# Optimization experiments

Measured on AMD Instinct MI355X. Metric: run time of the kernel, lower is better.

The kernel has to match this reference:

```python
import jax, jax.numpy as jnp
import numpy as np

TOPK_INC = 20  # top-k vertices per mention that form a hyperedge (torch.topk(attention_a, 20))
TOPK_OUT = 2   # top-k node reps concatenated into the output (torch.topk(X_score, k=2))


def _indicator_from_rows(att, idx):
    # att: [N, N], idx: [A] int. Rows with idx == 0 are skipped, as in the original loop.
    N = att.shape[0]
    rows = att[idx]                                   # [A, N] gather of attention rows
    _, top = jax.lax.top_k(rows, TOPK_INC)            # [A, TOPK_INC]
    mask = (idx != 0).astype(att.dtype)               # [A]
    vals = jnp.broadcast_to(mask[:, None], top.shape).reshape(-1)
    # scatter-max builds the 0/1 incidence vector (multiple mentions OR together)
    return jnp.zeros((N,), att.dtype).at[top.reshape(-1)].max(vals)  # [N]


def _forward_one(h, att, a_idx, b_idx, spk, W_w, W_b, S_w, S_b):
    # h: [N, H], att: [N, N], spk: [N] (single speaker row since speak_num == 1 -> E = 3)
    a_ind = _indicator_from_rows(att, a_idx)
    b_ind = _indicator_from_rows(att, b_idx)
    Hyper0 = jnp.stack([a_ind, b_ind, spk], axis=0)   # [E, N] binary incidence
    Dv = 1.0 / jnp.sqrt(Hyper0.sum(axis=0) + 1.0)     # sqrt(inverse(diag(Dv) + I)) diagonal, [N]
    De = 1.0 / jnp.sqrt(Hyper0.sum(axis=1))           # sqrt(inverse(diag(De))) diagonal, [E]
    Hyper = Hyper0 @ att                              # [E, N]  (dropout is identity in eval)
    Hyper_att = jax.nn.softmax(Hyper, axis=-1)        # F.softmax over last dim for 2D input
    Hyper_prime = Hyper_att @ h                       # [E, H]
    w = jax.nn.softmax(Hyper_prime @ W_w.T + W_b, axis=0)[:, 0]  # [E]
    # A = diag(Dv) @ Hyper0.T @ diag(w) @ diag(De) @ Hyper @ diag(Dv); X = A @ h.
    # Associate as M @ (K @ h) to avoid materializing the [N, N] matrix A.
    K = (w * De)[:, None] * Hyper * Dv[None, :]       # [E, N]
    M = Hyper0.T * Dv[:, None]                        # [N, E]
    X = M @ (K @ h)                                   # [N, H]
    score = (X @ S_w.T + S_b)[:, 0]                   # [N]
    _, top = jax.lax.top_k(score, TOPK_OUT)           # [2]
    return X[top].reshape(-1)                         # [2*H]


def setup_inputs() -> dict:
    key = jax.random.key(0)
    B, N, H, A = 32, 1024, 768, 8
    ks = jax.random.split(key, 8)
    inp = jax.random.normal(ks[0], (B, N, H), dtype=jnp.float32)
    word_att = jax.random.uniform(ks[1], (B, 1, N, N), dtype=jnp.float32)
    a_idx = jax.random.randint(ks[2], (B, A), 0, N)
    b_idx = jax.random.randint(ks[3], (B, A), 0, N)
    speak_num = jnp.ones((B, 1), dtype=jnp.int64 if jax.config.jax_enable_x64 else jnp.int32)
    speak_all = jax.random.randint(ks[4], (B, 3, N), 0, 2).astype(jnp.float32)
    W_w = jax.random.normal(ks[5], (1, H), dtype=jnp.float32) * (1.0 / np.sqrt(H))
    W_b = jnp.zeros((1,), dtype=jnp.float32)
    score_w = jax.random.normal(ks[6], (1, H), dtype=jnp.float32) * (1.0 / np.sqrt(H))
    score_b = jnp.zeros((1,), dtype=jnp.float32)
    return {"input": inp, "word_att": word_att, "a_idx": a_idx, "b_idx": b_idx,
            "speak_num": speak_num, "speak_all": speak_all,
            "W_w": W_w, "W_b": W_b, "score_w": score_w, "score_b": score_b}


def reference(input, word_att, a_idx, b_idx, speak_num, speak_all, W_w, W_b, score_w, score_b):
    # speak_num is all ones by construction -> exactly one speaker hyperedge per sample (E = 3)
    att = word_att[:, 0]           # [B, N, N]
    spk = speak_all[:, 0]          # [B, N]
    f = jax.vmap(_forward_one, in_axes=(0, 0, 0, 0, 0, None, None, None, None))
    return f(input, att, a_idx, b_idx, spk, W_w, W_b, score_w, score_b)  # [B, 2*H]
```

## Files before the change

### kernel.cpp

```cpp
#include <hip/hip_runtime.h>
#include <math.h>

#define B_ 32
#define N_ 1024
#define H_ 768
#define A_ 8
#define TOPK_ 20

__device__ __forceinline__ float wsum(float x) {
#pragma unroll
    for (int off = 32; off > 0; off >>= 1) x += __shfl_xor(x, off);
    return x;
}

__global__ __launch_bounds__(1024) void k1_ind(
    const float* __restrict__ att, const int* __restrict__ a_idx,
    const int* __restrict__ b_idx, const float* __restrict__ speak_all,
    float* __restrict__ aind, float* __restrict__ bind,
    float* __restrict__ Dv, float* __restrict__ De)
{
    const int b = blockIdx.x;
    const int tid = threadIdx.x;
    const int w = tid >> 6, lane = tid & 63;
    __shared__ float s_ind[2][N_];
    __shared__ float s_red[3][16];

    s_ind[0][tid] = 0.f;
    s_ind[1][tid] = 0.f;
    __syncthreads();

    const int which = w >> 3;
    const int r = w & 7;
    const int idx = which ? b_idx[b * A_ + r] : a_idx[b * A_ + r];
    if (idx != 0) {
        const float* row = att + ((size_t)b * N_ + idx) * N_;
        float v[16];
#pragma unroll
        for (int k = 0; k < 16; ++k) v[k] = row[(k << 6) + lane];
        float* dst = s_ind[which];
        for (int t = 0; t < TOPK_; ++t) {
            float bv = v[0]; int bk = 0;
#pragma unroll
            for (int k = 1; k < 16; ++k)
                if (v[k] > bv) { bv = v[k]; bk = k; }
            int bc = (bk << 6) + lane;
#pragma unroll
            for (int off = 32; off > 0; off >>= 1) {
                float ov = __shfl_xor(bv, off);
                int oc = __shfl_xor(bc, off);
                if (ov > bv || (ov == bv && oc < bc)) { bv = ov; bc = oc; }
            }
            if (lane == 0) dst[bc] = 1.f;
            if (lane == (bc & 63)) v[bc >> 6] = -INFINITY;
        }
    }
    __syncthreads();

    const float sa = s_ind[0][tid], sb = s_ind[1][tid];
    const float ss = speak_all[(size_t)b * 3 * N_ + tid];
    aind[b * N_ + tid] = sa;
    bind[b * N_ + tid] = sb;
    Dv[b * N_ + tid] = 1.f / sqrtf(sa + sb + ss + 1.f);

    float p[3] = {sa, sb, ss};
#pragma unroll
    for (int e = 0; e < 3; ++e) {
        float x = wsum(p[e]);
        if (lane == 0) s_red[e][w] = x;
    }
    __syncthreads();
    if (tid < 3) {
        float s = 0.f;
        for (int i = 0; i < 16; ++i) s += s_red[tid][i];
        De[b * 3 + tid] = 1.f / sqrtf(s);
    }
}

__global__ __launch_bounds__(256) void k2_hyper(
    const float* __restrict__ att, const float* __restrict__ aind,
    const float* __restrict__ bind, const float* __restrict__ speak_all,
    float* __restrict__ Hyper)
{
    const int b = blockIdx.y;
    const int col0 = blockIdx.x * 32;
    const int tid = threadIdx.x;
    const int cx = tid & 7, ry = tid >> 3;
    __shared__ float lds[256 * 13];
    float* w0 = lds;
    float* w1 = lds + N_;
    float* w2 = lds + 2 * N_;

    for (int n = tid; n < N_; n += 256) {
        w0[n] = aind[b * N_ + n];
        w1[n] = bind[b * N_ + n];
        w2[n] = speak_all[(size_t)b * 3 * N_ + n];
    }
    __syncthreads();

    float a0x=0,a0y=0,a0z=0,a0w=0, a1x=0,a1y=0,a1z=0,a1w=0, a2x=0,a2y=0,a2z=0,a2w=0;
    const float* base = att + (size_t)b * N_ * N_ + col0 + cx * 4;
    for (int n = ry; n < N_; n += 32) {
        const float x0 = w0[n], x1 = w1[n], x2 = w2[n];
        if (x0 == 0.f && x1 == 0.f && x2 == 0.f) continue;
        const float4 v = *(const float4*)(base + (size_t)n * N_);
        a0x += x0*v.x; a0y += x0*v.y; a0z += x0*v.z; a0w += x0*v.w;
        a1x += x1*v.x; a1y += x1*v.y; a1z += x1*v.z; a1w += x1*v.w;
        a2x += x2*v.x; a2y += x2*v.y; a2z += x2*v.z; a2w += x2*v.w;
    }
    __syncthreads();

    float vals[12] = {a0x,a0y,a0z,a0w, a1x,a1y,a1z,a1w, a2x,a2y,a2z,a2w};
    float* scr = lds;
#pragma unroll
    for (int k = 0; k < 12; ++k) scr[tid * 13 + k] = vals[k];
    __syncthreads();
    for (int s = 16; s > 0; s >>= 1) {
        if (ry < s) {
#pragma unroll
            for (int k = 0; k < 12; ++k)
                scr[tid * 13 + k] += scr[(tid + s * 8) * 13 + k];
        }
        __syncthreads();
    }
    if (ry == 0) {
#pragma unroll
        for (int e = 0; e < 3; ++e)
#pragma unroll
            for (int j = 0; j < 4; ++j)
                Hyper[(size_t)(b * 3 + e) * N_ + col0 + cx * 4 + j] = scr[tid * 13 + e * 4 + j];
    }
}

__global__ __launch_bounds__(256) void k4_ug(
    const float* __restrict__ h, const float* __restrict__ Hyper,
    const float* __restrict__ Dv, float* __restrict__ U, float* __restrict__ G)
{
    const int b = blockIdx.y;
    const int col0 = blockIdx.x * 32;
    const int tid = threadIdx.x;
    const int cx = tid & 7, ry = tid >> 3;
    const int lane = tid & 63, wv = tid >> 6;
    __shared__ float lds[256 * 25];
    float* sH = lds;
    float* sDv = lds + 3 * N_;
    float* rscr = lds + 4 * N_;

    for (int n = tid; n < N_; n += 256) {
        sDv[n] = Dv[b * N_ + n];
#pragma unroll
        for (int e = 0; e < 3; ++e)
            sH[e * N_ + n] = Hyper[(size_t)(b * 3 + e) * N_ + n];
    }
    __syncthreads();

    float m0 = -INFINITY, m1 = -INFINITY, m2 = -INFINITY;
    for (int n = tid; n < N_; n += 256) {
        m0 = fmaxf(m0, sH[n]); m1 = fmaxf(m1, sH[N_ + n]); m2 = fmaxf(m2, sH[2 * N_ + n]);
    }
#pragma unroll
    for (int off = 32; off > 0; off >>= 1) {
        m0 = fmaxf(m0, __shfl_xor(m0, off));
        m1 = fmaxf(m1, __shfl_xor(m1, off));
        m2 = fmaxf(m2, __shfl_xor(m2, off));
    }
    if (lane == 0) { rscr[wv * 3 + 0] = m0; rscr[wv * 3 + 1] = m1; rscr[wv * 3 + 2] = m2; }
    __syncthreads();
    m0 = fmaxf(fmaxf(rscr[0], rscr[3]), fmaxf(rscr[6], rscr[9]));
    m1 = fmaxf(fmaxf(rscr[1], rscr[4]), fmaxf(rscr[7], rscr[10]));
    m2 = fmaxf(fmaxf(rscr[2], rscr[5]), fmaxf(rscr[8], rscr[11]));
    __syncthreads();
    float s0 = 0.f, s1 = 0.f, s2 = 0.f;
    for (int n = tid; n < N_; n += 256) {
        s0 += expf(sH[n] - m0); s1 += expf(sH[N_ + n] - m1); s2 += expf(sH[2 * N_ + n] - m2);
    }
    s0 = wsum(s0); s1 = wsum(s1); s2 = wsum(s2);
    if (lane == 0) { rscr[wv * 3 + 0] = s0; rscr[wv * 3 + 1] = s1; rscr[wv * 3 + 2] = s2; }
    __syncthreads();
    const float iZ0 = 1.f / (rscr[0] + rscr[3] + rscr[6] + rscr[9]);
    const float iZ1 = 1.f / (rscr[1] + rscr[4] + rscr[7] + rscr[10]);
    const float iZ2 = 1.f / (rscr[2] + rscr[5] + rscr[8] + rscr[11]);
    __syncthreads();

    float u0x=0,u0y=0,u0z=0,u0w=0, u1x=0,u1y=0,u1z=0,u1w=0, u2x=0,u2y=0,u2z=0,u2w=0;
    float g0x=0,g0y=0,g0z=0,g0w=0, g1x=0,g1y=0,g1z=0,g1w=0, g2x=0,g2y=0,g2z=0,g2w=0;
    const float* base = h + (size_t)b * N_ * H_ + col0 + cx * 4;
    for (int n = ry; n < N_; n += 32) {
        const float H0 = sH[n], H1 = sH[N_ + n], H2 = sH[2 * N_ + n];
        const float dv = sDv[n];
        const float w0 = expf(H0 - m0) * iZ0;
        const float w1 = expf(H1 - m1) * iZ1;
        const float w2 = expf(H2 - m2) * iZ2;
        const float gg0 = H0 * dv, gg1 = H1 * dv, gg2 = H2 * dv;
        const float4 v = *(const float4*)(base + (size_t)n * H_);
        u0x += w0*v.x; u0y += w0*v.y; u0z += w0*v.z; u0w += w0*v.w;
        u1x += w1*v.x; u1y += w1*v.y; u1z += w1*v.z; u1w += w1*v.w;
        u2x += w2*v.x; u2y += w2*v.y; u2z += w2*v.z; u2w += w2*v.w;
        g0x += gg0*v.x; g0y += gg0*v.y; g0z += gg0*v.z; g0w += gg0*v.w;
        g1x += gg1*v.x; g1y += gg1*v.y; g1z += gg1*v.z; g1w += gg1*v.w;
        g2x += gg2*v.x; g2y += gg2*v.y; g2z += gg2*v.z; g2w += gg2*v.w;
    }
    __syncthreads();

    float vals[24] = {u0x,u0y,u0z,u0w, u1x,u1y,u1z,u1w, u2x,u2y,u2z,u2w,
                      g0x,g0y,g0z,g0w, g1x,g1y,g1z,g1w, g2x,g2y,g2z,g2w};
    float* scr = lds;
#pragma unroll
    for (int k = 0; k < 24; ++k) scr[tid * 25 + k] = vals[k];
    __syncthreads();
    for (int s = 16; s > 0; s >>= 1) {
        if (ry < s) {
#pragma unroll
            for (int k = 0; k < 24; ++k)
                scr[tid * 25 + k] += scr[(tid + s * 8) * 25 + k];
        }
        __syncthreads();
    }
    if (ry == 0) {
#pragma unroll
        for (int e = 0; e < 3; ++e)
#pragma unroll
            for (int j = 0; j < 4; ++j) {
                U[(size_t)(b * 3 + e) * H_ + col0 + cx * 4 + j] = scr[tid * 25 + e * 4 + j];
                G[(size_t)(b * 3 + e) * H_ + col0 + cx * 4 + j] = scr[tid * 25 + 12 + e * 4 + j];
            }
    }
}

__global__ __launch_bounds__(256) void k5_fin(
    const float* __restrict__ U, const float* __restrict__ G,
    const float* __restrict__ De, const float* __restrict__ Dv,
    const float* __restrict__ aind, const float* __restrict__ bind,
    const float* __restrict__ speak_all,
    const float* __restrict__ W_w, const float* __restrict__ W_b,
    const float* __restrict__ S_w, const float* __restrict__ S_b,
    float* __restrict__ out)
{
    const int b = blockIdx.x, tid = threadIdx.x;
    const int lane = tid & 63, wv = tid >> 6;
    __shared__ float sKh[3 * H_];
    __shared__ float sscore[N_];
    __shared__ float sred[16];
    __shared__ int sidx[4];

    const float* Ub = U + (size_t)b * 3 * H_;
    const float* Gb = G + (size_t)b * 3 * H_;

    float p0 = 0.f, p1 = 0.f, p2 = 0.f;
    for (int j = tid; j < H_; j += 256) {
        const float ww = W_w[j];
        p0 += Ub[j] * ww; p1 += Ub[H_ + j] * ww; p2 += Ub[2 * H_ + j] * ww;
    }
    p0 = wsum(p0); p1 = wsum(p1); p2 = wsum(p2);
    if (lane == 0) { sred[wv * 3 + 0] = p0; sred[wv * 3 + 1] = p1; sred[wv * 3 + 2] = p2; }
    __syncthreads();
    const float wb = W_b[0];
    const float l0 = sred[0] + sred[3] + sred[6] + sred[9]  + wb;
    const float l1 = sred[1] + sred[4] + sred[7] + sred[10] + wb;
    const float l2 = sred[2] + sred[5] + sred[8] + sred[11] + wb;
    const float mx = fmaxf(l0, fmaxf(l1, l2));
    const float e0 = expf(l0 - mx), e1 = expf(l1 - mx), e2 = expf(l2 - mx);
    const float inv = 1.f / (e0 + e1 + e2);
    const float wd0 = e0 * inv * De[b * 3 + 0];
    const float wd1 = e1 * inv * De[b * 3 + 1];
    const float wd2 = e2 * inv * De[b * 3 + 2];

    for (int j = tid; j < H_; j += 256) {
        sKh[j]          = wd0 * Gb[j];
        sKh[H_ + j]     = wd1 * Gb[H_ + j];
        sKh[2 * H_ + j] = wd2 * Gb[2 * H_ + j];
    }
    __syncthreads();

    float q0 = 0.f, q1 = 0.f, q2 = 0.f;
    for (int j = tid; j < H_; j += 256) {
        const float sw = S_w[j];
        q0 += sKh[j] * sw; q1 += sKh[H_ + j] * sw; q2 += sKh[2 * H_ + j] * sw;
    }
    q0 = wsum(q0); q1 = wsum(q1); q2 = wsum(q2);
    if (lane == 0) { sred[wv * 3 + 0] = q0; sred[wv * 3 + 1] = q1; sred[wv * 3 + 2] = q2; }
    __syncthreads();
    q0 = sred[0] + sred[3] + sred[6] + sred[9];
    q1 = sred[1] + sred[4] + sred[7] + sred[10];
    q2 = sred[2] + sred[5] + sred[8] + sred[11];

    const float sb0 = S_b[0];
    const float* av = aind + b * N_;
    const float* bv2 = bind + b * N_;
    const float* dv = Dv + b * N_;
    const float* sv = speak_all + (size_t)b * 3 * N_;
    for (int n = tid; n < N_; n += 256)
        sscore[n] = dv[n] * (av[n] * q0 + bv2[n] * q1 + sv[n] * q2) + sb0;
    __syncthreads();

    int r0;
    {
        float best = -INFINITY; int bi = N_;
        for (int n = tid; n < N_; n += 256) {
            const float s = sscore[n];
            if (s > best || (s == best && n < bi)) { best = s; bi = n; }
        }
#pragma unroll
        for (int off = 32; off > 0; off >>= 1) {
            const float ov = __shfl_xor(best, off); const int oi = __shfl_xor(bi, off);
            if (ov > best || (ov == best && oi < bi)) { best = ov; bi = oi; }
        }
        if (lane == 0) { sred[wv] = best; sidx[wv] = bi; }
        __syncthreads();
        float v = -INFINITY; int i = N_;
        for (int k = 0; k < 4; ++k)
            if (sred[k] > v || (sred[k] == v && sidx[k] < i)) { v = sred[k]; i = sidx[k]; }
        r0 = i;
    }
    __syncthreads();
    int r1;
    {
        float best = -INFINITY; int bi = N_;
        for (int n = tid; n < N_; n += 256) {
            if (n == r0) continue;
            const float s = sscore[n];
            if (s > best || (s == best && n < bi)) { best = s; bi = n; }
        }
#pragma unroll
        for (int off = 32; off > 0; off >>= 1) {
            const float ov = __shfl_xor(best, off); const int oi = __shfl_xor(bi, off);
            if (ov > best || (ov == best && oi < bi)) { best = ov; bi = oi; }
        }
        if (lane == 0) { sred[wv] = best; sidx[wv] = bi; }
        __syncthreads();
        float v = -INFINITY; int i = N_;
        for (int k = 0; k < 4; ++k)
            if (sred[k] > v || (sred[k] == v && sidx[k] < i)) { v = sred[k]; i = sidx[k]; }
        r1 = i;
    }

    float* ob = out + (size_t)b * 2 * H_;
    {
        const float d = dv[r0], wa = av[r0], wbn = bv2[r0], wsv = sv[r0];
        for (int j = tid; j < H_; j += 256)
            ob[j] = d * (wa * sKh[j] + wbn * sKh[H_ + j] + wsv * sKh[2 * H_ + j]);
    }
    {
        const float d = dv[r1], wa = av[r1], wbn = bv2[r1], wsv = sv[r1];
        for (int j = tid; j < H_; j += 256)
            ob[H_ + j] = d * (wa * sKh[j] + wbn * sKh[H_ + j] + wsv * sKh[2 * H_ + j]);
    }
}

extern "C" void kernel_launch(void* const* d_in, const int* in_sizes, int n_in,
                              void* d_out, int out_size, void* d_ws, size_t ws_size,
                              hipStream_t stream)
{
    const float* h         = (const float*)d_in[0];
    const float* att       = (const float*)d_in[1];
    const int*   a_idx     = (const int*)d_in[2];
    const int*   b_idx     = (const int*)d_in[3];
    const float* speak_all = (const float*)d_in[5];
    const float* W_w       = (const float*)d_in[6];
    const float* W_b       = (const float*)d_in[7];
    const float* S_w       = (const float*)d_in[8];
    const float* S_b       = (const float*)d_in[9];
    float* out = (float*)d_out;

    float* ws    = (float*)d_ws;
    float* aind  = ws;
    float* bind  = aind + B_ * N_;
    float* Dv    = bind + B_ * N_;
    float* De    = Dv + B_ * N_;
    float* Hyper = De + 128;
    float* U     = Hyper + B_ * 3 * N_;
    float* G     = U + B_ * 3 * H_;

    k1_ind<<<B_, 1024, 0, stream>>>(att, a_idx, b_idx, speak_all, aind, bind, Dv, De);
    k2_hyper<<<dim3(32, B_), 256, 0, stream>>>(att, aind, bind, speak_all, Hyper);
    k4_ug<<<dim3(24, B_), 256, 0, stream>>>(h, Hyper, Dv, U, G);
    k5_fin<<<B_, 256, 0, stream>>>(U, G, De, Dv, aind, bind, speak_all, W_w, W_b, S_w, S_b, out);
}
```

Before: 80.34 us.

## Split reductions over N into row-chunk partials with separate reduce kernels

Replaces the column-tiled Hyper and U/G kernels with split-K style kernels. Each block handles a 64-row chunk of N across all columns and writes partial sums, and small reduction kernels (k3_wgg, k4b_red) combine them. k2 compacts the active rows with a ballot so it loads only nonzero-weight rows, and k3 computes the softmax weights and Dv scaling once instead of per column tile. This removes the in-block LDS tree reductions and redundant exp work, at the cost of two extra launches and partial-buffer traffic through global memory.

Result: no change. 81.49 us (+1.4%).

```diff
diff --git a/kernel.cpp b/kernel.cpp
--- a/kernel.cpp
+++ b/kernel.cpp
@@ -6,6 +6,8 @@
 #define H_ 768
 #define A_ 8
 #define TOPK_ 20
+#define CH2_ 16
+#define CH4_ 16
 
 __device__ __forceinline__ float wsum(float x) {
 #pragma unroll
@@ -76,154 +78,143 @@
     }
 }
 
-__global__ __launch_bounds__(256) void k2_hyper(
+__global__ __launch_bounds__(256) void k2_part(
     const float* __restrict__ att, const float* __restrict__ aind,
     const float* __restrict__ bind, const float* __restrict__ speak_all,
-    float* __restrict__ Hyper)
-{
-    const int b = blockIdx.y;
-    const int col0 = blockIdx.x * 32;
-    const int tid = threadIdx.x;
-    const int cx = tid & 7, ry = tid >> 3;
-    __shared__ float lds[256 * 13];
-    float* w0 = lds;
-    float* w1 = lds + N_;
-    float* w2 = lds + 2 * N_;
-
-    for (int n = tid; n < N_; n += 256) {
-        w0[n] = aind[b * N_ + n];
-        w1[n] = bind[b * N_ + n];
-        w2[n] = speak_all[(size_t)b * 3 * N_ + n];
-    }
-    __syncthreads();
+    float* __restrict__ Hpart)
+{
+    const int b = blockIdx.y, c = blockIdx.x;
+    const int n0 = c * 64;
+    const int t = threadIdx.x;
+    __shared__ float sw[3][64];
+    __shared__ int rows[64];
+    __shared__ int s_nr;
+
+    if (t < 192) {
+        const int e = t >> 6, r = t & 63, n = n0 + r;
+        float v;
+        if (e == 0)      v = aind[b * N_ + n];
+        else if (e == 1) v = bind[b * N_ + n];
+        else             v = speak_all[(size_t)b * 3 * N_ + n];
+        sw[e][r] = v;
+    }
+    __syncthreads();
+    if (t < 64) {
+        const bool act = (sw[0][t] != 0.f) || (sw[1][t] != 0.f) || (sw[2][t] != 0.f);
+        const unsigned long long m = __ballot(act);
+        if (act) rows[__popcll(m & ((1ull << t) - 1ull))] = t;
+        if (t == 0) s_nr = (int)__popcll(m);
+    }
+    __syncthreads();
+    const int nr = s_nr;
 
     float a0x=0,a0y=0,a0z=0,a0w=0, a1x=0,a1y=0,a1z=0,a1w=0, a2x=0,a2y=0,a2z=0,a2w=0;
-    const float* base = att + (size_t)b * N_ * N_ + col0 + cx * 4;
-    for (int n = ry; n < N_; n += 32) {
-        const float x0 = w0[n], x1 = w1[n], x2 = w2[n];
-        if (x0 == 0.f && x1 == 0.f && x2 == 0.f) continue;
-        const float4 v = *(const float4*)(base + (size_t)n * N_);
+    const float* base = att + (size_t)b * N_ * N_ + (size_t)n0 * N_ + t * 4;
+#pragma unroll 2
+    for (int i = 0; i < nr; ++i) {
+        const int r = rows[i];
+        const float x0 = sw[0][r], x1 = sw[1][r], x2 = sw[2][r];
+        const float4 v = *(const float4*)(base + (size_t)r * N_);
         a0x += x0*v.x; a0y += x0*v.y; a0z += x0*v.z; a0w += x0*v.w;
         a1x += x1*v.x; a1y += x1*v.y; a1z += x1*v.z; a1w += x1*v.w;
         a2x += x2*v.x; a2y += x2*v.y; a2z += x2*v.z; a2w += x2*v.w;
     }
-    __syncthreads();
-
-    float vals[12] = {a0x,a0y,a0z,a0w, a1x,a1y,a1z,a1w, a2x,a2y,a2z,a2w};
-    float* scr = lds;
-#pragma unroll
-    for (int k = 0; k < 12; ++k) scr[tid * 13 + k] = vals[k];
-    __syncthreads();
-    for (int s = 16; s > 0; s >>= 1) {
-        if (ry < s) {
-#pragma unroll
-            for (int k = 0; k < 12; ++k)
-                scr[tid * 13 + k] += scr[(tid + s * 8) * 13 + k];
-        }
-        __syncthreads();
-    }
-    if (ry == 0) {
-#pragma unroll
-        for (int e = 0; e < 3; ++e)
-#pragma unroll
-            for (int j = 0; j < 4; ++j)
-                Hyper[(size_t)(b * 3 + e) * N_ + col0 + cx * 4 + j] = scr[tid * 13 + e * 4 + j];
-    }
-}
-
-__global__ __launch_bounds__(256) void k4_ug(
-    const float* __restrict__ h, const float* __restrict__ Hyper,
-    const float* __restrict__ Dv, float* __restrict__ U, float* __restrict__ G)
-{
-    const int b = blockIdx.y;
-    const int col0 = blockIdx.x * 32;
-    const int tid = threadIdx.x;
-    const int cx = tid & 7, ry = tid >> 3;
-    const int lane = tid & 63, wv = tid >> 6;
-    __shared__ float lds[256 * 25];
-    float* sH = lds;
-    float* sDv = lds + 3 * N_;
-    float* rscr = lds + 4 * N_;
-
-    for (int n = tid; n < N_; n += 256) {
-        sDv[n] = Dv[b * N_ + n];
-#pragma unroll
-        for (int e = 0; e < 3; ++e)
-            sH[e * N_ + n] = Hyper[(size_t)(b * 3 + e) * N_ + n];
-    }
-    __syncthreads();
-
-    float m0 = -INFINITY, m1 = -INFINITY, m2 = -INFINITY;
-    for (int n = tid; n < N_; n += 256) {
-        m0 = fmaxf(m0, sH[n]); m1 = fmaxf(m1, sH[N_ + n]); m2 = fmaxf(m2, sH[2 * N_ + n]);
-    }
-#pragma unroll
-    for (int off = 32; off > 0; off >>= 1) {
-        m0 = fmaxf(m0, __shfl_xor(m0, off));
-        m1 = fmaxf(m1, __shfl_xor(m1, off));
-        m2 = fmaxf(m2, __shfl_xor(m2, off));
-    }
-    if (lane == 0) { rscr[wv * 3 + 0] = m0; rscr[wv * 3 + 1] = m1; rscr[wv * 3 + 2] = m2; }
-    __syncthreads();
-    m0 = fmaxf(fmaxf(rscr[0], rscr[3]), fmaxf(rscr[6], rscr[9]));
-    m1 = fmaxf(fmaxf(rscr[1], rscr[4]), fmaxf(rscr[7], rscr[10]));
-    m2 = fmaxf(fmaxf(rscr[2], rscr[5]), fmaxf(rscr[8], rscr[11]));
-    __syncthreads();
-    float s0 = 0.f, s1 = 0.f, s2 = 0.f;
-    for (int n = tid; n < N_; n += 256) {
-        s0 += expf(sH[n] - m0); s1 += expf(sH[N_ + n] - m1); s2 += expf(sH[2 * N_ + n] - m2);
-    }
-    s0 = wsum(s0); s1 = wsum(s1); s2 = wsum(s2);
-    if (lane == 0) { rscr[wv * 3 + 0] = s0; rscr[wv * 3 + 1] = s1; rscr[wv * 3 + 2] = s2; }
-    __syncthreads();
-    const float iZ0 = 1.f / (rscr[0] + rscr[3] + rscr[6] + rscr[9]);
-    const float iZ1 = 1.f / (rscr[1] + rscr[4] + rscr[7] + rscr[10]);
-    const float iZ2 = 1.f / (rscr[2] + rscr[5] + rscr[8] + rscr[11]);
+    float* hp = Hpart + (size_t)(b * CH2_ + c) * 3 * N_ + t * 4;
+    *(float4*)(hp)          = make_float4(a0x, a0y, a0z, a0w);
+    *(float4*)(hp + N_)     = make_float4(a1x, a1y, a1z, a1w);
+    *(float4*)(hp + 2 * N_) = make_float4(a2x, a2y, a2z, a2w);
+}
+
+__global__ __launch_bounds__(256) void k3_wgg(
+    const float* __restrict__ Hpart, const float* __restrict__ Dv,
+    float* __restrict__ wArr, float* __restrict__ ggArr)
+{
+    const int e = blockIdx.x, b = blockIdx.y;
+    const int t = threadIdx.x;
+    const int lane = t & 63, wv = t >> 6;
+    __shared__ float sred[4];
+
+    float4 acc = make_float4(0.f, 0.f, 0.f, 0.f);
+    for (int c = 0; c < CH2_; ++c) {
+        const float4 v = *(const float4*)(Hpart + ((size_t)(b * CH2_ + c) * 3 + e) * N_ + t * 4);
+        acc.x += v.x; acc.y += v.y; acc.z += v.z; acc.w += v.w;
+    }
+    float m = fmaxf(fmaxf(acc.x, acc.y), fmaxf(acc.z, acc.w));
+#pragma unroll
+    for (int off = 32; off > 0; off >>= 1) m = fmaxf(m, __shfl_xor(m, off));
+    if (lane == 0) sred[wv] = m;
+    __syncthreads();
+    m = fmaxf(fmaxf(sred[0], sred[1]), fmaxf(sred[2], sred[3]));
+    __syncthreads();
+    float z = __expf(acc.x - m) + __expf(acc.y - m) + __expf(acc.z - m) + __expf(acc.w - m);
+    z = wsum(z);
+    if (lane == 0) sred[wv] = z;
+    __syncthreads();
+    const float iZ = 1.f / (sred[0] + sred[1] + sred[2] + sred[3]);
+
+    const float4 dv = *(const float4*)(Dv + b * N_ + t * 4);
+    float4 w4 = make_float4(__expf(acc.x - m) * iZ, __expf(acc.y - m) * iZ,
+                            __expf(acc.z - m) * iZ, __expf(acc.w - m) * iZ);
+    float4 g4 = make_float4(acc.x * dv.x, acc.y * dv.y, acc.z * dv.z, acc.w * dv.w);
+    *(float4*)(wArr  + ((size_t)(b * 3 + e)) * N_ + t * 4) = w4;
+    *(float4*)(ggArr + ((size_t)(b * 3 + e)) * N_ + t * 4) = g4;
+}
+
+__global__ __launch_bounds__(192) void k4_part(
+    const float* __restrict__ h, const float* __restrict__ wArr,
+    const float* __restrict__ ggArr, float* __restrict__ UGpart)
+{
+    const int b = blockIdx.y, c = blockIdx.x;
+    const int n0 = c * 64;
+    const int t = threadIdx.x;
+    __shared__ float sw[6][64];
+    for (int i = t; i < 384; i += 192) {
+        const int s = i >> 6, r = i & 63;
+        sw[s][r] = (s < 3) ? wArr[((size_t)(b * 3 + s)) * N_ + n0 + r]
+                           : ggArr[((size_t)(b * 3 + s - 3)) * N_ + n0 + r];
+    }
     __syncthreads();
 
     float u0x=0,u0y=0,u0z=0,u0w=0, u1x=0,u1y=0,u1z=0,u1w=0, u2x=0,u2y=0,u2z=0,u2w=0;
     float g0x=0,g0y=0,g0z=0,g0w=0, g1x=0,g1y=0,g1z=0,g1w=0, g2x=0,g2y=0,g2z=0,g2w=0;
-    const float* base = h + (size_t)b * N_ * H_ + col0 + cx * 4;
-    for (int n = ry; n < N_; n += 32) {
-        const float H0 = sH[n], H1 = sH[N_ + n], H2 = sH[2 * N_ + n];
-        const float dv = sDv[n];
-        const float w0 = expf(H0 - m0) * iZ0;
-        const float w1 = expf(H1 - m1) * iZ1;
-        const float w2 = expf(H2 - m2) * iZ2;
-        const float gg0 = H0 * dv, gg1 = H1 * dv, gg2 = H2 * dv;
-        const float4 v = *(const float4*)(base + (size_t)n * H_);
+    const float* base = h + (size_t)b * N_ * H_ + (size_t)n0 * H_ + t * 4;
+#pragma unroll 4
+    for (int r = 0; r < 64; ++r) {
+        const float4 v = *(const float4*)(base + (size_t)r * H_);
+        const float w0 = sw[0][r], w1 = sw[1][r], w2 = sw[2][r];
+        const float g0 = sw[3][r], g1 = sw[4][r], g2 = sw[5][r];
         u0x += w0*v.x; u0y += w0*v.y; u0z += w0*v.z; u0w += w0*v.w;
         u1x += w1*v.x; u1y += w1*v.y; u1z += w1*v.z; u1w += w1*v.w;
         u2x += w2*v.x; u2y += w2*v.y; u2z += w2*v.z; u2w += w2*v.w;
-        g0x += gg0*v.x; g0y += gg0*v.y; g0z += gg0*v.z; g0w += gg0*v.w;
-        g1x += gg1*v.x; g1y += gg1*v.y; g1z += gg1*v.z; g1w += gg1*v.w;
-        g2x += gg2*v.x; g2y += gg2*v.y; g2z += gg2*v.z; g2w += gg2*v.w;
-    }
-    __syncthreads();
-
-    float vals[24] = {u0x,u0y,u0z,u0w, u1x,u1y,u1z,u1w, u2x,u2y,u2z,u2w,
-                      g0x,g0y,g0z,g0w, g1x,g1y,g1z,g1w, g2x,g2y,g2z,g2w};
-    float* scr = lds;
-#pragma unroll
-    for (int k = 0; k < 24; ++k) scr[tid * 25 + k] = vals[k];
-    __syncthreads();
-    for (int s = 16; s > 0; s >>= 1) {
-        if (ry < s) {
-#pragma unroll
-            for (int k = 0; k < 24; ++k)
-                scr[tid * 25 + k] += scr[(tid + s * 8) * 25 + k];
-        }
-        __syncthreads();
-    }
-    if (ry == 0) {
-#pragma unroll
-        for (int e = 0; e < 3; ++e)
-#pragma unroll
-            for (int j = 0; j < 4; ++j) {
-                U[(size_t)(b * 3 + e) * H_ + col0 + cx * 4 + j] = scr[tid * 25 + e * 4 + j];
-                G[(size_t)(b * 3 + e) * H_ + col0 + cx * 4 + j] = scr[tid * 25 + 12 + e * 4 + j];
-            }
-    }
+        g0x += g0*v.x; g0y += g0*v.y; g0z += g0*v.z; g0w += g0*v.w;
+        g1x += g1*v.x; g1y += g1*v.y; g1z += g1*v.z; g1w += g1*v.w;
+        g2x += g2*v.x; g2y += g2*v.y; g2z += g2*v.z; g2w += g2*v.w;
+    }
+    float* up = UGpart + (size_t)(b * CH4_ + c) * 6 * H_ + t * 4;
+    *(float4*)(up)          = make_float4(u0x, u0y, u0z, u0w);
+    *(float4*)(up + H_)     = make_float4(u1x, u1y, u1z, u1w);
+    *(float4*)(up + 2*H_)   = make_float4(u2x, u2y, u2z, u2w);
+    *(float4*)(up + 3*H_)   = make_float4(g0x, g0y, g0z, g0w);
+    *(float4*)(up + 4*H_)   = make_float4(g1x, g1y, g1z, g1w);
+    *(float4*)(up + 5*H_)   = make_float4(g2x, g2y, g2z, g2w);
+}
+
+__global__ __launch_bounds__(256) void k4b_red(
+    const float* __restrict__ UGpart, float* __restrict__ U, float* __restrict__ G)
+{
+    const int gid = blockIdx.x * 256 + threadIdx.x;
+    const int b = gid / 1152;
+    const int rem = gid % 1152;
+    const int s = rem / 192;
+    const int col = (rem % 192) * 4;
+
+    float4 acc = make_float4(0.f, 0.f, 0.f, 0.f);
+    for (int c = 0; c < CH4_; ++c) {
+        const float4 v = *(const float4*)(UGpart + (size_t)(b * CH4_ + c) * 6 * H_ + s * H_ + col);
+        acc.x += v.x; acc.y += v.y; acc.z += v.z; acc.w += v.w;
+    }
+    if (s < 3) *(float4*)(U + ((size_t)(b * 3 + s)) * H_ + col) = acc;
+    else       *(float4*)(G + ((size_t)(b * 3 + s - 3)) * H_ + col) = acc;
 }
 
 __global__ __launch_bounds__(256) void k5_fin(
@@ -273,8 +264,8 @@
 
     float q0 = 0.f, q1 = 0.f, q2 = 0.f;
     for (int j = tid; j < H_; j += 256) {
-        const float sw = S_w[j];
-        q0 += sKh[j] * sw; q1 += sKh[H_ + j] * sw; q2 += sKh[2 * H_ + j] * sw;
+        const float sw2 = S_w[j];
+        q0 += sKh[j] * sw2; q1 += sKh[H_ + j] * sw2; q2 += sKh[2 * H_ + j] * sw2;
     }
     q0 = wsum(q0); q1 = wsum(q1); q2 = wsum(q2);
     if (lane == 0) { sred[wv * 3 + 0] = q0; sred[wv * 3 + 1] = q1; sred[wv * 3 + 2] = q2; }
@@ -361,17 +352,22 @@
     const float* S_b       = (const float*)d_in[9];
     float* out = (float*)d_out;
 
-    float* ws    = (float*)d_ws;
-    float* aind  = ws;
-    float* bind  = aind + B_ * N_;
-    float* Dv    = bind + B_ * N_;
-    float* De    = Dv + B_ * N_;
-    float* Hyper = De + 128;
-    float* U     = Hyper + B_ * 3 * N_;
-    float* G     = U + B_ * 3 * H_;
+    float* ws     = (float*)d_ws;
+    float* aind   = ws;
+    float* bind   = aind + B_ * N_;
+    float* Dv     = bind + B_ * N_;
+    float* De     = Dv + B_ * N_;
+    float* Hpart  = De + 128;
+    float* wArr   = Hpart + B_ * CH2_ * 3 * N_;
+    float* ggArr  = wArr + B_ * 3 * N_;
+    float* UGpart = ggArr + B_ * 3 * N_;
+    float* U      = UGpart + B_ * CH4_ * 6 * H_;
+    float* G      = U + B_ * 3 * H_;
 
     k1_ind<<<B_, 1024, 0, stream>>>(att, a_idx, b_idx, speak_all, aind, bind, Dv, De);
-    k2_hyper<<<dim3(32, B_), 256, 0, stream>>>(att, aind, bind, speak_all, Hyper);
-    k4_ug<<<dim3(24, B_), 256, 0, stream>>>(h, Hyper, Dv, U, G);
+    k2_part<<<dim3(CH2_, B_), 256, 0, stream>>>(att, aind, bind, speak_all, Hpart);
+    k3_wgg<<<dim3(3, B_), 256, 0, stream>>>(Hpart, Dv, wArr, ggArr);
+    k4_part<<<dim3(CH4_, B_), 192, 0, stream>>>(h, wArr, ggArr, UGpart);
+    k4b_red<<<144, 256, 0, stream>>>(UGpart, U, G);
     k5_fin<<<B_, 256, 0, stream>>>(U, G, De, Dv, aind, bind, speak_all, W_w, W_b, S_w, S_b, out);
 }
```

## Split h-projection kernel over row chunks with partial sums reduced in final kernel

Applied to the files above, without the earlier changes.

The U/G projection kernel now gives each block 64 rows of h across the full hidden width, instead of 32 columns across all 1024 rows. Each thread reads contiguous float4s along a row, and the LDS tree reduction is dropped. Per-block partial results go to a workspace buffer, and the final kernel sums the 16 chunks before the scoring epilogue. This is meant to improve coalescing of the dominant h read and remove reduction and sync overhead. In exchange it adds partial-sum traffic through global memory and recomputes the softmax statistics redundantly in every block.

New measurement: 83.27 us. +3.7%, slower.

```diff
diff --git a/kernel.cpp b/kernel.cpp
--- a/kernel.cpp
+++ b/kernel.cpp
@@ -6,6 +6,7 @@
 #define H_ 768
 #define A_ 8
 #define TOPK_ 20
+#define CH4_ 16
 
 __device__ __forceinline__ float wsum(float x) {
 #pragma unroll
@@ -85,10 +86,8 @@
     const int col0 = blockIdx.x * 32;
     const int tid = threadIdx.x;
     const int cx = tid & 7, ry = tid >> 3;
-    __shared__ float lds[256 * 13];
-    float* w0 = lds;
-    float* w1 = lds + N_;
-    float* w2 = lds + 2 * N_;
+    __shared__ float w0[N_], w1[N_], w2[N_];
+    __shared__ float scr[256 * 13];
 
     for (int n = tid; n < N_; n += 256) {
         w0[n] = aind[b * N_ + n];
@@ -110,7 +109,6 @@
     __syncthreads();
 
     float vals[12] = {a0x,a0y,a0z,a0w, a1x,a1y,a1z,a1w, a2x,a2y,a2z,a2w};
-    float* scr = lds;
 #pragma unroll
     for (int k = 0; k < 12; ++k) scr[tid * 13 + k] = vals[k];
     __syncthreads();
@@ -131,103 +129,69 @@
     }
 }
 
-__global__ __launch_bounds__(256) void k4_ug(
+__global__ __launch_bounds__(192) void k4_ug(
     const float* __restrict__ h, const float* __restrict__ Hyper,
-    const float* __restrict__ Dv, float* __restrict__ U, float* __restrict__ G)
-{
-    const int b = blockIdx.y;
-    const int col0 = blockIdx.x * 32;
-    const int tid = threadIdx.x;
-    const int cx = tid & 7, ry = tid >> 3;
-    const int lane = tid & 63, wv = tid >> 6;
-    __shared__ float lds[256 * 25];
-    float* sH = lds;
-    float* sDv = lds + 3 * N_;
-    float* rscr = lds + 4 * N_;
-
-    for (int n = tid; n < N_; n += 256) {
-        sDv[n] = Dv[b * N_ + n];
-#pragma unroll
-        for (int e = 0; e < 3; ++e)
-            sH[e * N_ + n] = Hyper[(size_t)(b * 3 + e) * N_ + n];
-    }
-    __syncthreads();
-
-    float m0 = -INFINITY, m1 = -INFINITY, m2 = -INFINITY;
-    for (int n = tid; n < N_; n += 256) {
-        m0 = fmaxf(m0, sH[n]); m1 = fmaxf(m1, sH[N_ + n]); m2 = fmaxf(m2, sH[2 * N_ + n]);
-    }
-#pragma unroll
-    for (int off = 32; off > 0; off >>= 1) {
-        m0 = fmaxf(m0, __shfl_xor(m0, off));
-        m1 = fmaxf(m1, __shfl_xor(m1, off));
-        m2 = fmaxf(m2, __shfl_xor(m2, off));
-    }
-    if (lane == 0) { rscr[wv * 3 + 0] = m0; rscr[wv * 3 + 1] = m1; rscr[wv * 3 + 2] = m2; }
-    __syncthreads();
-    m0 = fmaxf(fmaxf(rscr[0], rscr[3]), fmaxf(rscr[6], rscr[9]));
-    m1 = fmaxf(fmaxf(rscr[1], rscr[4]), fmaxf(rscr[7], rscr[10]));
-    m2 = fmaxf(fmaxf(rscr[2], rscr[5]), fmaxf(rscr[8], rscr[11]));
-    __syncthreads();
-    float s0 = 0.f, s1 = 0.f, s2 = 0.f;
-    for (int n = tid; n < N_; n += 256) {
-        s0 += expf(sH[n] - m0); s1 += expf(sH[N_ + n] - m1); s2 += expf(sH[2 * N_ + n] - m2);
-    }
-    s0 = wsum(s0); s1 = wsum(s1); s2 = wsum(s2);
-    if (lane == 0) { rscr[wv * 3 + 0] = s0; rscr[wv * 3 + 1] = s1; rscr[wv * 3 + 2] = s2; }
-    __syncthreads();
-    const float iZ0 = 1.f / (rscr[0] + rscr[3] + rscr[6] + rscr[9]);
-    const float iZ1 = 1.f / (rscr[1] + rscr[4] + rscr[7] + rscr[10]);
-    const float iZ2 = 1.f / (rscr[2] + rscr[5] + rscr[8] + rscr[11]);
+    const float* __restrict__ Dv, float* __restrict__ UGpart)
+{
+    const int b = blockIdx.y, c = blockIdx.x;
+    const int n0 = c * 64;
+    const int t = threadIdx.x;
+    const int wv = t >> 6, lane = t & 63;
+    __shared__ float sH[3 * N_];
+    __shared__ float sw[6][64];
+    __shared__ float smz[6];
+
+    for (int i = t; i < 3 * N_; i += 192)
+        sH[i] = Hyper[(size_t)b * 3 * N_ + i];
+    __syncthreads();
+
+    {
+        const float* He = sH + wv * N_;
+        float m = -INFINITY;
+        for (int n = lane; n < N_; n += 64) m = fmaxf(m, He[n]);
+#pragma unroll
+        for (int off = 32; off > 0; off >>= 1) m = fmaxf(m, __shfl_xor(m, off));
+        float z = 0.f;
+        for (int n = lane; n < N_; n += 64) z += expf(He[n] - m);
+        z = wsum(z);
+        if (lane == 0) { smz[wv] = m; smz[3 + wv] = 1.f / z; }
+    }
+    __syncthreads();
+
+    {
+        const int e = t >> 6, r = t & 63;
+        const float Hv = sH[e * N_ + n0 + r];
+        sw[e][r] = expf(Hv - smz[e]) * smz[3 + e];
+        sw[3 + e][r] = Hv * Dv[b * N_ + n0 + r];
+    }
     __syncthreads();
 
     float u0x=0,u0y=0,u0z=0,u0w=0, u1x=0,u1y=0,u1z=0,u1w=0, u2x=0,u2y=0,u2z=0,u2w=0;
     float g0x=0,g0y=0,g0z=0,g0w=0, g1x=0,g1y=0,g1z=0,g1w=0, g2x=0,g2y=0,g2z=0,g2w=0;
-    const float* base = h + (size_t)b * N_ * H_ + col0 + cx * 4;
-    for (int n = ry; n < N_; n += 32) {
-        const float H0 = sH[n], H1 = sH[N_ + n], H2 = sH[2 * N_ + n];
-        const float dv = sDv[n];
-        const float w0 = expf(H0 - m0) * iZ0;
-        const float w1 = expf(H1 - m1) * iZ1;
-        const float w2 = expf(H2 - m2) * iZ2;
-        const float gg0 = H0 * dv, gg1 = H1 * dv, gg2 = H2 * dv;
-        const float4 v = *(const float4*)(base + (size_t)n * H_);
+    const float* base = h + (size_t)b * N_ * H_ + (size_t)n0 * H_ + t * 4;
+#pragma unroll 8
+    for (int r = 0; r < 64; ++r) {
+        const float4 v = *(const float4*)(base + (size_t)r * H_);
+        const float w0 = sw[0][r], w1 = sw[1][r], w2 = sw[2][r];
+        const float g0 = sw[3][r], g1 = sw[4][r], g2 = sw[5][r];
         u0x += w0*v.x; u0y += w0*v.y; u0z += w0*v.z; u0w += w0*v.w;
         u1x += w1*v.x; u1y += w1*v.y; u1z += w1*v.z; u1w += w1*v.w;
         u2x += w2*v.x; u2y += w2*v.y; u2z += w2*v.z; u2w += w2*v.w;
-        g0x += gg0*v.x; g0y += gg0*v.y; g0z += gg0*v.z; g0w += gg0*v.w;
-        g1x += gg1*v.x; g1y += gg1*v.y; g1z += gg1*v.z; g1w += gg1*v.w;
-        g2x += gg2*v.x; g2y += gg2*v.y; g2z += gg2*v.z; g2w += gg2*v.w;
-    }
-    __syncthreads();
-
-    float vals[24] = {u0x,u0y,u0z,u0w, u1x,u1y,u1z,u1w, u2x,u2y,u2z,u2w,
-                      g0x,g0y,g0z,g0w, g1x,g1y,g1z,g1w, g2x,g2y,g2z,g2w};
-    float* scr = lds;
-#pragma unroll
-    for (int k = 0; k < 24; ++k) scr[tid * 25 + k] = vals[k];
-    __syncthreads();
-    for (int s = 16; s > 0; s >>= 1) {
-        if (ry < s) {
-#pragma unroll
-            for (int k = 0; k < 24; ++k)
-                scr[tid * 25 + k] += scr[(tid + s * 8) * 25 + k];
-        }
-        __syncthreads();
-    }
-    if (ry == 0) {
-#pragma unroll
-        for (int e = 0; e < 3; ++e)
-#pragma unroll
-            for (int j = 0; j < 4; ++j) {
-                U[(size_t)(b * 3 + e) * H_ + col0 + cx * 4 + j] = scr[tid * 25 + e * 4 + j];
-                G[(size_t)(b * 3 + e) * H_ + col0 + cx * 4 + j] = scr[tid * 25 + 12 + e * 4 + j];
-            }
-    }
-}
-
-__global__ __launch_bounds__(256) void k5_fin(
-    const float* __restrict__ U, const float* __restrict__ G,
+        g0x += g0*v.x; g0y += g0*v.y; g0z += g0*v.z; g0w += g0*v.w;
+        g1x += g1*v.x; g1y += g1*v.y; g1z += g1*v.z; g1w += g1*v.w;
+        g2x += g2*v.x; g2y += g2*v.y; g2z += g2*v.z; g2w += g2*v.w;
+    }
+    float* up = UGpart + (size_t)(b * CH4_ + c) * 6 * H_ + t * 4;
+    *(float4*)(up)          = make_float4(u0x, u0y, u0z, u0w);
+    *(float4*)(up + H_)     = make_float4(u1x, u1y, u1z, u1w);
+    *(float4*)(up + 2*H_)   = make_float4(u2x, u2y, u2z, u2w);
+    *(float4*)(up + 3*H_)   = make_float4(g0x, g0y, g0z, g0w);
+    *(float4*)(up + 4*H_)   = make_float4(g1x, g1y, g1z, g1w);
+    *(float4*)(up + 5*H_)   = make_float4(g2x, g2y, g2z, g2w);
+}
+
+__global__ __launch_bounds__(256) void k45_fin(
+    const float* __restrict__ UGpart,
     const float* __restrict__ De, const float* __restrict__ Dv,
     const float* __restrict__ aind, const float* __restrict__ bind,
     const float* __restrict__ speak_all,
@@ -237,13 +201,34 @@
 {
     const int b = blockIdx.x, tid = threadIdx.x;
     const int lane = tid & 63, wv = tid >> 6;
+    __shared__ float sUG[6 * H_];
     __shared__ float sKh[3 * H_];
     __shared__ float sscore[N_];
     __shared__ float sred[16];
     __shared__ int sidx[4];
 
-    const float* Ub = U + (size_t)b * 3 * H_;
-    const float* Gb = G + (size_t)b * 3 * H_;
+    {
+        const float* p = UGpart + (size_t)b * CH4_ * 6 * H_;
+        for (int slot = tid; slot < 1152; slot += 256) {
+            const int off = slot * 4;
+            float4 a0 = make_float4(0.f, 0.f, 0.f, 0.f);
+            float4 a1 = make_float4(0.f, 0.f, 0.f, 0.f);
+            for (int c = 0; c < CH4_; c += 2) {
+                const float4 v0 = *(const float4*)(p + (size_t)c * 6 * H_ + off);
+                const float4 v1 = *(const float4*)(p + (size_t)(c + 1) * 6 * H_ + off);
+                a0.x += v0.x; a0.y += v0.y; a0.z += v0.z; a0.w += v0.w;
+                a1.x += v1.x; a1.y += v1.y; a1.z += v1.z; a1.w += v1.w;
+            }
+            sUG[off + 0] = a0.x + a1.x;
+            sUG[off + 1] = a0.y + a1.y;
+            sUG[off + 2] = a0.z + a1.z;
+            sUG[off + 3] = a0.w + a1.w;
+        }
+    }
+    __syncthreads();
+
+    const float* Ub = sUG;
+    const float* Gb = sUG + 3 * H_;
 
     float p0 = 0.f, p1 = 0.f, p2 = 0.f;
     for (int j = tid; j < H_; j += 256) {
@@ -263,6 +248,7 @@
     const float wd0 = e0 * inv * De[b * 3 + 0];
     const float wd1 = e1 * inv * De[b * 3 + 1];
     const float wd2 = e2 * inv * De[b * 3 + 2];
+    __syncthreads();
 
     for (int j = tid; j < H_; j += 256) {
         sKh[j]          = wd0 * Gb[j];
@@ -273,8 +259,8 @@
 
     float q0 = 0.f, q1 = 0.f, q2 = 0.f;
     for (int j = tid; j < H_; j += 256) {
-        const float sw = S_w[j];
-        q0 += sKh[j] * sw; q1 += sKh[H_ + j] * sw; q2 += sKh[2 * H_ + j] * sw;
+        const float sw2 = S_w[j];
+        q0 += sKh[j] * sw2; q1 += sKh[H_ + j] * sw2; q2 += sKh[2 * H_ + j] * sw2;
     }
     q0 = wsum(q0); q1 = wsum(q1); q2 = wsum(q2);
     if (lane == 0) { sred[wv * 3 + 0] = q0; sred[wv * 3 + 1] = q1; sred[wv * 3 + 2] = q2; }
@@ -361,17 +347,16 @@
     const float* S_b       = (const float*)d_in[9];
     float* out = (float*)d_out;
 
-    float* ws    = (float*)d_ws;
-    float* aind  = ws;
-    float* bind  = aind + B_ * N_;
-    float* Dv    = bind + B_ * N_;
-    float* De    = Dv + B_ * N_;
-    float* Hyper = De + 128;
-    float* U     = Hyper + B_ * 3 * N_;
-    float* G     = U + B_ * 3 * H_;
+    float* ws     = (float*)d_ws;
+    float* aind   = ws;
+    float* bind   = aind + B_ * N_;
+    float* Dv     = bind + B_ * N_;
+    float* De     = Dv + B_ * N_;
+    float* Hyper  = De + 128;
+    float* UGpart = Hyper + B_ * 3 * N_;
 
     k1_ind<<<B_, 1024, 0, stream>>>(att, a_idx, b_idx, speak_all, aind, bind, Dv, De);
     k2_hyper<<<dim3(32, B_), 256, 0, stream>>>(att, aind, bind, speak_all, Hyper);
-    k4_ug<<<dim3(24, B_), 256, 0, stream>>>(h, Hyper, Dv, U, G);
-    k5_fin<<<B_, 256, 0, stream>>>(U, G, De, Dv, aind, bind, speak_all, W_w, W_b, S_w, S_b, out);
-}
+    k4_ug<<<dim3(CH4_, B_), 192, 0, stream>>>(h, Hyper, Dv, UGpart);
+    k45_fin<<<B_, 256, 0, stream>>>(UGpart, De, Dv, aind, bind, speak_all, W_w, W_b, S_w, S_b, out);
+}
```
